# Performance work log

Measured on AMD Instinct MI355X. Metric: run time of the kernel, lower is better.

The kernel has to match this reference:

```python
import jax, jax.numpy as jnp
import numpy as np

WS = 7  # window_size
SHIFT = 3  # shift_size
NH = 4  # num_heads
EPS = 1e-5


def layer_norm(x, g, b):
    mu = jnp.mean(x, axis=-1, keepdims=True)
    var = jnp.mean(jnp.square(x - mu), axis=-1, keepdims=True)
    return (x - mu) * jax.lax.rsqrt(var + EPS) * g + b


def setup_inputs() -> dict:
    key = jax.random.key(0)
    ks = jax.random.split(key, 12)
    B, H, W, C = 64, 56, 56, 128
    hid = int(C * 3.0)
    s = lambda fan: 1.0 / np.sqrt(fan)
    return {
        "x": jax.random.normal(ks[0], (B, H * W, C), jnp.float32),
        "g1": jnp.ones((C,), jnp.float32),
        "be1": jnp.zeros((C,), jnp.float32),
        "Wqkv": jax.random.normal(ks[1], (3 * C, C), jnp.float32) * s(C),
        "bqkv": jnp.zeros((3 * C,), jnp.float32),
        "Wproj": jax.random.normal(ks[2], (C, C), jnp.float32) * s(C),
        "bproj": jnp.zeros((C,), jnp.float32),
        "g2": jnp.ones((C,), jnp.float32),
        "be2": jnp.zeros((C,), jnp.float32),
        "Wm1": jax.random.normal(ks[3], (hid, C), jnp.float32) * s(C),
        "bm1": jnp.zeros((hid,), jnp.float32),
        "Wm2": jax.random.normal(ks[4], (C, hid), jnp.float32) * s(hid),
        "bm2": jnp.zeros((C,), jnp.float32),
        "H": 56,
        "W": 56,
    }


def reference(x, g1, be1, Wqkv, bqkv, Wproj, bproj, g2, be2, Wm1, bm1, Wm2, bm2, H, W):
    B, L, C = x.shape
    shortcut = x
    h = layer_norm(x, g1, be1).reshape(B, H, W, C)
    if SHIFT > 0:
        h = jnp.roll(h, shift=(-SHIFT, -SHIFT), axis=(1, 2))
    pad_h = (WS - H % WS) % WS
    pad_w = (WS - W % WS) % WS
    if pad_h or pad_w:
        h = jnp.pad(h, ((0, 0), (0, pad_h), (0, pad_w), (0, 0)))
    Hp, Wp = H + pad_h, W + pad_w
    # window partition: [B*nW, WS*WS, C]
    h = h.reshape(B, Hp // WS, WS, Wp // WS, WS, C)
    h = h.transpose(0, 1, 3, 2, 4, 5).reshape(-1, WS * WS, C)
    # windowed attention (mask=None, matching original)
    Bw, N, _ = h.shape
    d = C // NH
    qkv = (h @ Wqkv.T + bqkv).reshape(Bw, N, 3, NH, d).transpose(2, 0, 3, 1, 4)
    q, k, v = qkv[0], qkv[1], qkv[2]  # [Bw, NH, N, d]
    attn = jax.nn.softmax(jnp.einsum('whnd,whmd->whnm', q, k) * (d ** -0.5), axis=-1)
    o = jnp.einsum('whnm,whmd->whnd', attn, v).transpose(0, 2, 1, 3).reshape(Bw, N, C)
    o = o @ Wproj.T + bproj
    # window reverse
    o = o.reshape(B, Hp // WS, Wp // WS, WS, WS, C)
    o = o.transpose(0, 1, 3, 2, 4, 5).reshape(B, Hp, Wp, C)
    if pad_h or pad_w:
        o = o[:, :H, :W, :]
    if SHIFT > 0:
        o = jnp.roll(o, shift=(SHIFT, SHIFT), axis=(1, 2))
    h = shortcut + o.reshape(B, H * W, C)
    # MLP with residual
    m = layer_norm(h, g2, be2)
    m = jax.nn.gelu(m @ Wm1.T + bm1, approximate=False) @ Wm2.T + bm2
    return h + m
```

## Files before the change

### kernel.cpp

```cpp
#include <hip/hip_runtime.h>
#include <hip/hip_bf16.h>
#include <cstdint>

typedef short bf16x8 __attribute__((ext_vector_type(8)));
typedef float f32x4 __attribute__((ext_vector_type(4)));

constexpr int Bn = 64, Hn = 56, Wn = 56, Cn = 128, Ln = 3136;
constexpr int NWIN = 4096;
constexpr int NTOK = 49;
constexpr int Mtot = NWIN * NTOK;
constexpr int HID = 384;
constexpr int SHIFT_ = 3;

__device__ __forceinline__ float bf2f(short s) {
  union { uint32_t u; float f; } c; c.u = ((uint32_t)(uint16_t)s) << 16; return c.f;
}
__device__ __forceinline__ short f2bf(float f) {
  union { float f; uint32_t u; } c; c.f = f;
  uint32_t r = (c.u + 0x7FFFu + ((c.u >> 16) & 1u)) >> 16;
  return (short)r;
}
__device__ __forceinline__ float wred(float v) {
  #pragma unroll
  for (int o = 32; o > 0; o >>= 1) v += __shfl_xor(v, o);
  return v;
}

__device__ __forceinline__ size_t plain_off(int m, int l15) {
  int win = m / NTOK, tok = m - win * NTOK;
  int b = win >> 6, wi = win & 63;
  int hr = (wi >> 3) * 7 + tok / 7 + SHIFT_; if (hr >= Hn) hr -= Hn;
  int wr = (wi & 7) * 7 + tok % 7 + SHIFT_;  if (wr >= Wn) wr -= Wn;
  return (size_t)(b * Ln + hr * Wn + wr) * Cn + l15;
}

__global__ void k_cvt4(const float* __restrict__ s0, const float* __restrict__ s1,
                       const float* __restrict__ s2, const float* __restrict__ s3,
                       short* __restrict__ d0, short* __restrict__ d1,
                       short* __restrict__ d2, short* __restrict__ d3) {
  int i = blockIdx.x * 256 + threadIdx.x;
  if (i < 49152) d0[i] = f2bf(s0[i]);
  else if (i < 65536) d1[i - 49152] = f2bf(s1[i - 49152]);
  else if (i < 114688) d2[i - 65536] = f2bf(s2[i - 65536]);
  else if (i < 163840) d3[i - 114688] = f2bf(s3[i - 114688]);
}

__global__ __launch_bounds__(256) void k_ln1(const float* __restrict__ x,
                                             const float* __restrict__ g,
                                             const float* __restrict__ be,
                                             short* __restrict__ out) {
  int wave = threadIdx.x >> 6, lane = threadIdx.x & 63;
  int row = blockIdx.x * 4 + wave;
  int win = row / NTOK, tok = row % NTOK;
  int b = win >> 6, wi = win & 63;
  int wh = wi >> 3, ww = wi & 7;
  int hr = wh * 7 + tok / 7;
  int wr = ww * 7 + tok % 7;
  int hs = hr + SHIFT_; if (hs >= Hn) hs -= Hn;
  int ws2 = wr + SHIFT_; if (ws2 >= Wn) ws2 -= Wn;
  const float* xr = x + (size_t)(b * Ln + hs * Wn + ws2) * Cn;
  float2 v = *(const float2*)(xr + lane * 2);
  float sum = wred(v.x + v.y);
  float sq  = wred(v.x * v.x + v.y * v.y);
  float mean = sum * (1.f / Cn);
  float var  = sq * (1.f / Cn) - mean * mean;
  float rstd = rsqrtf(var + 1e-5f);
  int c0 = lane * 2;
  short2 o;
  o.x = f2bf((v.x - mean) * rstd * g[c0]     + be[c0]);
  o.y = f2bf((v.y - mean) * rstd * g[c0 + 1] + be[c0 + 1]);
  *(short2*)(out + (size_t)row * Cn + c0) = o;
}

__global__ __launch_bounds__(512) void k_qkvg(const short* __restrict__ A,
                                              const short* __restrict__ W,
                                              const float* __restrict__ bias,
                                              short* __restrict__ outB) {
  __shared__ __attribute__((aligned(16))) short sW[64 * 128];
  const int t = threadIdx.x;
  const int wave = t >> 6, lane = t & 63;
  const int l15 = lane & 15, gq = lane >> 4;
  const int m_base = blockIdx.x * 128;
  const int wrow = wave * 16;
  const int kb = gq * 8;

  bf16x8 af[4];
  #pragma unroll
  for (int s = 0; s < 4; ++s)
    af[s] = *(const bf16x8*)(A + (size_t)(m_base + wrow + l15) * Cn + s * 32 + kb);

  short* b0[4];
  #pragma unroll
  for (int r = 0; r < 4; ++r) {
    int m = m_base + wrow + 4 * gq + r;
    int win = m / NTOK, tok = m - win * NTOK;
    b0[r] = outB + ((size_t)win * 3 * NTOK + tok) * Cn + l15;
  }

  #pragma unroll
  for (int nb = 0; nb < 6; ++nb) {
    __syncthreads();
    #pragma unroll
    for (int i = 0; i < 2; ++i) {
      int idx = i * 512 + t;
      int n = idx >> 4, gr = idx & 15;
      *(bf16x8*)(&sW[n * 128 + ((gr ^ (n & 7)) << 3)]) =
          *(const bf16x8*)(W + (size_t)(nb * 64 + n) * Cn + gr * 8);
    }
    __syncthreads();

    f32x4 acc[4];
    #pragma unroll
    for (int tt = 0; tt < 4; ++tt) acc[tt] = (f32x4){0.f, 0.f, 0.f, 0.f};
    #pragma unroll
    for (int s = 0; s < 4; ++s) {
      #pragma unroll
      for (int tt = 0; tt < 4; ++tt) {
        bf16x8 bfr = *(const bf16x8*)(&sW[(tt * 16 + l15) * 128 +
                                          (((s * 4 + gq) ^ (l15 & 7)) << 3)]);
        acc[tt] = __builtin_amdgcn_mfma_f32_16x16x32_bf16(af[s], bfr, acc[tt], 0, 0, 0);
      }
    }

    #pragma unroll
    for (int tt = 0; tt < 4; ++tt) {
      const int colc = nb * 64 + tt * 16;
      float bv = bias[colc + l15];
      #pragma unroll
      for (int r = 0; r < 4; ++r) {
        float v = acc[tt][r] + bv;
        b0[r][((colc >> 7) * NTOK * Cn) + (colc & 127)] = f2bf(v);
      }
    }
  }
}

__global__ __launch_bounds__(512) void k_mlp(const short* __restrict__ A,
                                             const short* __restrict__ W1,
                                             const float* __restrict__ b1,
                                             const short* __restrict__ W2,
                                             const float* __restrict__ b2,
                                             float* __restrict__ outF) {
  __shared__ __attribute__((aligned(16))) short sW1[64 * 128];
  __shared__ __attribute__((aligned(16))) short sW2[128 * 64];
  __shared__ __attribute__((aligned(16))) short sAct[128 * 64];
  const int t = threadIdx.x;
  const int wave = t >> 6, lane = t & 63;
  const int l15 = lane & 15, gq = lane >> 4;
  const int m_base = blockIdx.x * 128;
  const int wrow = wave * 16;
  const int kb = gq * 8;

  bf16x8 af[4];
  #pragma unroll
  for (int s = 0; s < 4; ++s)
    af[s] = *(const bf16x8*)(A + (size_t)(m_base + wrow + l15) * Cn + s * 32 + kb);

  f32x4 acc2[8];
  #pragma unroll
  for (int tt = 0; tt < 8; ++tt) acc2[tt] = (f32x4){0.f, 0.f, 0.f, 0.f};

  for (int nb = 0; nb < 6; ++nb) {
    __syncthreads();
    #pragma unroll
    for (int i = 0; i < 2; ++i) {
      int idx = i * 512 + t;
      int n = idx >> 4, gr = idx & 15;
      *(bf16x8*)(&sW1[n * 128 + ((gr ^ (n & 7)) << 3)]) =
          *(const bf16x8*)(W1 + (size_t)(nb * 64 + n) * Cn + gr * 8);
    }
    #pragma unroll
    for (int i = 0; i < 2; ++i) {
      int idx = i * 512 + t;
      int n = idx >> 3, gr = idx & 7;
      *(bf16x8*)(&sW2[n * 64 + ((gr ^ (n & 7)) << 3)]) =
          *(const bf16x8*)(W2 + (size_t)n * HID + nb * 64 + gr * 8);
    }
    __syncthreads();

    f32x4 acc1[4];
    #pragma unroll
    for (int tt = 0; tt < 4; ++tt) acc1[tt] = (f32x4){0.f, 0.f, 0.f, 0.f};
    #pragma unroll
    for (int s = 0; s < 4; ++s) {
      #pragma unroll
      for (int tt = 0; tt < 4; ++tt) {
        bf16x8 bfr = *(const bf16x8*)(&sW1[(tt * 16 + l15) * 128 +
                                           (((s * 4 + gq) ^ (l15 & 7)) << 3)]);
        acc1[tt] = __builtin_amdgcn_mfma_f32_16x16x32_bf16(af[s], bfr, acc1[tt], 0, 0, 0);
      }
    }
    #pragma unroll
    for (int tt = 0; tt < 4; ++tt) {
      float bb = b1[nb * 64 + tt * 16 + l15];
      #pragma unroll
      for (int r = 0; r < 4; ++r) {
        float v = acc1[tt][r] + bb;
        float e = __expf(-1.702f * v);
        float gg = v * __builtin_amdgcn_rcpf(1.f + e);
        int arow = wrow + 4 * gq + r;
        int col = tt * 16 + l15;
        sAct[arow * 64 + (((col >> 3) ^ (arow & 7)) << 3) + (col & 7)] = f2bf(gg);
      }
    }
    bf16x8 af2[2];
    #pragma unroll
    for (int sl = 0; sl < 2; ++sl)
      af2[sl] = *(const bf16x8*)(&sAct[(wrow + l15) * 64 +
                                       (((sl * 4 + gq) ^ (l15 & 7)) << 3)]);
    #pragma unroll
    for (int sl = 0; sl < 2; ++sl) {
      #pragma unroll
      for (int tt = 0; tt < 8; ++tt) {
        bf16x8 bfr = *(const bf16x8*)(&sW2[(tt * 16 + l15) * 64 +
                                           (((sl * 4 + gq) ^ (l15 & 7)) << 3)]);
        acc2[tt] = __builtin_amdgcn_mfma_f32_16x16x32_bf16(af2[sl], bfr, acc2[tt], 0, 0, 0);
      }
    }
  }

  float bb[8];
  #pragma unroll
  for (int tt = 0; tt < 8; ++tt) bb[tt] = b2[tt * 16 + l15];
  #pragma unroll
  for (int r = 0; r < 4; ++r) {
    int m = m_base + wrow + 4 * gq + r;
    float* p = outF + (size_t)m * Cn + l15;
    #pragma unroll
    for (int tt = 0; tt < 8; ++tt)
      p[tt * 16] = p[tt * 16] + acc2[tt][r] + bb[tt];
  }
}

__global__ __launch_bounds__(256) void k_proj(const short* __restrict__ A,
                                              const short* __restrict__ W,
                                              const float* __restrict__ bias,
                                              const float* __restrict__ x,
                                              const float* __restrict__ g2,
                                              const float* __restrict__ be2,
                                              float* __restrict__ hOut,
                                              short* __restrict__ lnOut) {
  __shared__ __attribute__((aligned(16))) short ldsW[128 * 128];
  const int t = threadIdx.x;
  const int wave = t >> 6, lane = t & 63;
  const int l15 = lane & 15, g = lane >> 4;
  const int m_base = blockIdx.x * 64 + wave * 16;
  const int kb = g * 8;

  size_t off[4];
  float xv[4][8];
  #pragma unroll
  for (int r = 0; r < 4; ++r) {
    int m = m_base + 4 * g + r;
    off[r] = plain_off(m, l15);
    #pragma unroll
    for (int c = 0; c < 8; ++c) xv[r][c] = x[off[r] + c * 16];
  }

  float bv[8], gv[8], bev[8];
  #pragma unroll
  for (int c = 0; c < 8; ++c) {
    bv[c] = bias[c * 16 + l15]; gv[c] = g2[c * 16 + l15]; bev[c] = be2[c * 16 + l15];
  }

  const int arow = m_base + l15;
  const int awin = arow / NTOK, atok = arow - awin * NTOK;
  const short* abase = A + (size_t)awin * 3 * NTOK * Cn + (size_t)atok * Cn;
  bf16x8 af[4];
  #pragma unroll
  for (int s = 0; s < 4; ++s)
    af[s] = *(const bf16x8*)(abase + s * 32 + kb);

  #pragma unroll
  for (int i = 0; i < 8; ++i) {
    int idx = i * 256 + t;
    int n = idx >> 4, gr = idx & 15;
    *(bf16x8*)(&ldsW[n * 128 + ((gr ^ (n & 7)) << 3)]) =
        *(const bf16x8*)(W + (size_t)n * Cn + gr * 8);
  }
  __syncthreads();

  f32x4 acc[8];
  #pragma unroll
  for (int tt = 0; tt < 8; ++tt) acc[tt] = (f32x4){0.f, 0.f, 0.f, 0.f};
  #pragma unroll
  for (int s = 0; s < 4; ++s) {
    #pragma unroll
    for (int tt = 0; tt < 8; ++tt) {
      int row = tt * 16 + l15;
      bf16x8 bfr = *(const bf16x8*)(&ldsW[row * 128 + (((s * 4 + g) ^ (l15 & 7)) << 3)]);
      acc[tt] = __builtin_amdgcn_mfma_f32_16x16x32_bf16(af[s], bfr, acc[tt], 0, 0, 0);
    }
  }

  #pragma unroll
  for (int r = 0; r < 4; ++r) {
    float hv[8];
    float s1 = 0.f, s2 = 0.f;
    #pragma unroll
    for (int tt = 0; tt < 8; ++tt) {
      hv[tt] = acc[tt][r] + bv[tt] + xv[r][tt];
      s1 += hv[tt];
      s2 += hv[tt] * hv[tt];
    }
    #pragma unroll
    for (int o = 8; o >= 1; o >>= 1) { s1 += __shfl_xor(s1, o); s2 += __shfl_xor(s2, o); }
    float mean = s1 * (1.f / Cn);
    float var  = s2 * (1.f / Cn) - mean * mean;
    float rstd = rsqrtf(var + 1e-5f);
    #pragma unroll
    for (int tt = 0; tt < 8; ++tt) {
      hOut[off[r] + tt * 16] = hv[tt];
      lnOut[off[r] + tt * 16] = f2bf((hv[tt] - mean) * rstd * gv[tt] + bev[tt]);
    }
  }
}

__global__ __launch_bounds__(256, 3) void k_attn(const short* __restrict__ qkv,
                                                 short* __restrict__ out) {
  __shared__ __attribute__((aligned(16))) short sVT[8192];
  __shared__ __attribute__((aligned(16))) short sP[4][4096];
  const int t = threadIdx.x;
  const int wave = t >> 6, lane = t & 63;
  const int l15 = lane & 15, g = lane >> 4;
  const int h = wave;
  const int win = blockIdx.x;
  const short* baseQ = qkv + (size_t)win * 3 * NTOK * Cn;
  const short* baseK = baseQ + NTOK * Cn;
  const short* baseV = baseK + NTOK * Cn;

  for (int i = t; i < NTOK * 16; i += 256) {
    int j = i >> 4, cb = (i & 15) * 8;
    int jj = j >> 3, u = j & 7;
    bf16x8 v = *(const bf16x8*)(baseV + (size_t)j * Cn + cb);
    #pragma unroll
    for (int uu = 0; uu < 8; ++uu) {
      int c = cb + uu;
      sVT[(c >> 4) * 1024 + (c & 15) * 64 + ((jj ^ (c & 7)) << 3) + u] = v[uu];
    }
  }
  for (int i = t; i < 128 * 15; i += 256) {
    int c = i / 15, j = 49 + i % 15;
    sVT[(c >> 4) * 1024 + (c & 15) * 64 + (((j >> 3) ^ (c & 7)) << 3) + (j & 7)] = 0;
  }

  bf16x8 aq[4], bk[4];
  #pragma unroll
  for (int mi = 0; mi < 4; ++mi)
    aq[mi] = *(const bf16x8*)(baseQ + (size_t)(mi * 16 + l15) * Cn + h * 32 + g * 8);
  #pragma unroll
  for (int ni = 0; ni < 4; ++ni)
    bk[ni] = *(const bf16x8*)(baseK + (size_t)(ni * 16 + l15) * Cn + h * 32 + g * 8);

  f32x4 s[4][4];
  #pragma unroll
  for (int mi = 0; mi < 4; ++mi)
    #pragma unroll
    for (int ni = 0; ni < 4; ++ni) {
      s[mi][ni] = (f32x4){0.f, 0.f, 0.f, 0.f};
      s[mi][ni] = __builtin_amdgcn_mfma_f32_16x16x32_bf16(aq[mi], bk[ni], s[mi][ni], 0, 0, 0);
    }

  const float SC = 0.17677669529663687f;
  #pragma unroll
  for (int mi = 0; mi < 4; ++mi) {
    #pragma unroll
    for (int r = 0; r < 4; ++r) {
      float a0 = s[mi][0][r] * SC, a1 = s[mi][1][r] * SC, a2 = s[mi][2][r] * SC;
      float a3 = (l15 == 0) ? s[mi][3][r] * SC : -1e30f;
      float m = fmaxf(fmaxf(a0, a1), fmaxf(a2, a3));
      #pragma unroll
      for (int o = 8; o >= 1; o >>= 1) m = fmaxf(m, __shfl_xor(m, o));
      float e0 = __expf(a0 - m), e1 = __expf(a1 - m), e2 = __expf(a2 - m);
      float e3 = (l15 == 0) ? __expf(a3 - m) : 0.f;
      float ss = e0 + e1 + e2 + e3;
      #pragma unroll
      for (int o = 8; o >= 1; o >>= 1) ss += __shfl_xor(ss, o);
      float inv = 1.f / ss;
      int rr = 4 * g + r;
      float ee[4] = {e0, e1, e2, e3};
      #pragma unroll
      for (int ni = 0; ni < 4; ++ni) {
        int col = 16 * ni + l15;
        sP[wave][(mi * 2 + (col >> 5)) * 512 + rr * 32 + (((col >> 3) & 3) * 8) + (col & 7)]
            = f2bf(ee[ni] * inv);
      }
    }
  }

  __syncthreads();

  f32x4 o_[4][2];
  #pragma unroll
  for (int mi = 0; mi < 4; ++mi)
    #pragma unroll
    for (int ni = 0; ni < 2; ++ni) o_[mi][ni] = (f32x4){0.f, 0.f, 0.f, 0.f};

  #pragma unroll
  for (int ks = 0; ks < 2; ++ks) {
    bf16x8 bv[2];
    #pragma unroll
    for (int ni = 0; ni < 2; ++ni)
      bv[ni] = *(const bf16x8*)(&sVT[(h * 2 + ni) * 1024 + l15 * 64 +
                                     (((ks * 4 + g) ^ (l15 & 7)) << 3)]);
    #pragma unroll
    for (int mi = 0; mi < 4; ++mi) {
      bf16x8 ap = *(const bf16x8*)(&sP[wave][(mi * 2 + ks) * 512 + l15 * 32 + g * 8]);
      #pragma unroll
      for (int ni = 0; ni < 2; ++ni)
        o_[mi][ni] = __builtin_amdgcn_mfma_f32_16x16x32_bf16(ap, bv[ni], o_[mi][ni], 0, 0, 0);
    }
  }

  #pragma unroll
  for (int mi = 0; mi < 4; ++mi) {
    #pragma unroll
    for (int r = 0; r < 4; ++r) {
      int i = 16 * mi + 4 * g + r;
      if (i < NTOK) {
        short* orow = out + ((size_t)win * 3 * NTOK + i) * Cn + h * 32;
        #pragma unroll
        for (int ni = 0; ni < 2; ++ni)
          orow[16 * ni + l15] = f2bf(o_[mi][ni][r]);
      }
    }
  }
}

extern "C" void kernel_launch(void* const* d_in, const int* in_sizes, int n_in,
                              void* d_out, int out_size, void* d_ws, size_t ws_size,
                              hipStream_t stream) {
  const float* x     = (const float*)d_in[0];
  const float* g1    = (const float*)d_in[1];
  const float* be1   = (const float*)d_in[2];
  const float* Wqkv  = (const float*)d_in[3];
  const float* bqkv  = (const float*)d_in[4];
  const float* Wproj = (const float*)d_in[5];
  const float* bproj = (const float*)d_in[6];
  const float* g2    = (const float*)d_in[7];
  const float* be2   = (const float*)d_in[8];
  const float* Wm1   = (const float*)d_in[9];
  const float* bm1   = (const float*)d_in[10];
  const float* Wm2   = (const float*)d_in[11];
  const float* bm2   = (const float*)d_in[12];
  float* out = (float*)d_out;

  char* ws = (char*)d_ws;
  size_t SA = (size_t)Mtot * Cn * 2;
  size_t SB = (size_t)Mtot * HID * 2;
  short* bufA = (short*)ws;
  short* bufB = (short*)(ws + SA);
  short* wq = (short*)(ws + SA + SB);
  short* wp = wq + 384 * 128;
  short* w1 = wp + 128 * 128;
  short* w2 = w1 + 384 * 128;

  k_cvt4<<<640, 256, 0, stream>>>(Wqkv, Wproj, Wm1, Wm2, wq, wp, w1, w2);

  k_ln1<<<Mtot / 4, 256, 0, stream>>>(x, g1, be1, bufA);
  k_qkvg<<<Mtot / 128, 512, 0, stream>>>(bufA, wq, bqkv, bufB);
  k_attn<<<NWIN, 256, 0, stream>>>(bufB, bufB);
  k_proj<<<Mtot / 64, 256, 0, stream>>>(bufB, wp, bproj, x, g2, be2, out, bufA);
  k_mlp<<<Mtot / 128, 512, 0, stream>>>(bufA, w1, bm1, w2, bm2, out);
}
```

Measured before the change: 322.1 us.

## Fuse projection, residual, LayerNorm2 and MLP into one kernel

Merges the attention output projection (with residual add and second LayerNorm) into the MLP kernel. The normalized activations stay in LDS and the residual stays in registers, so the fp32 h tensor and the bf16 LN tensor no longer make a round trip through global memory. The block now needs 80 KB of LDS and more registers (hv[4][8]), which may lower occupancy.

```diff
diff --git a/kernel.cpp b/kernel.cpp
--- a/kernel.cpp
+++ b/kernel.cpp
@@ -135,15 +135,23 @@
   }
 }
 
-__global__ __launch_bounds__(512) void k_mlp(const short* __restrict__ A,
-                                             const short* __restrict__ W1,
-                                             const float* __restrict__ b1,
-                                             const short* __restrict__ W2,
-                                             const float* __restrict__ b2,
-                                             float* __restrict__ outF) {
-  __shared__ __attribute__((aligned(16))) short sW1[64 * 128];
-  __shared__ __attribute__((aligned(16))) short sW2[128 * 64];
-  __shared__ __attribute__((aligned(16))) short sAct[128 * 64];
+__global__ __launch_bounds__(512) void k_projmlp(const short* __restrict__ A,
+                                                 const short* __restrict__ Wp,
+                                                 const float* __restrict__ bp,
+                                                 const float* __restrict__ x,
+                                                 const float* __restrict__ g2,
+                                                 const float* __restrict__ be2,
+                                                 const short* __restrict__ W1,
+                                                 const float* __restrict__ b1,
+                                                 const short* __restrict__ W2,
+                                                 const float* __restrict__ b2,
+                                                 float* __restrict__ outF) {
+  __shared__ __attribute__((aligned(16))) short lds[40960];
+  short* sWp  = lds;
+  short* sLn  = lds;
+  short* sW1  = lds + 16384;
+  short* sW2  = lds + 24576;
+  short* sAct = lds + 32768;
   const int t = threadIdx.x;
   const int wave = t >> 6, lane = t & 63;
   const int l15 = lane & 15, gq = lane >> 4;
@@ -151,10 +159,82 @@
   const int wrow = wave * 16;
   const int kb = gq * 8;
 
+  size_t off[4];
+  float xv[4][8];
+  #pragma unroll
+  for (int r = 0; r < 4; ++r) {
+    int m = m_base + wrow + 4 * gq + r;
+    off[r] = plain_off(m, l15);
+    #pragma unroll
+    for (int c = 0; c < 8; ++c) xv[r][c] = x[off[r] + c * 16];
+  }
+  float bpv[8], gv[8], bev[8];
+  #pragma unroll
+  for (int c = 0; c < 8; ++c) {
+    bpv[c] = bp[c * 16 + l15]; gv[c] = g2[c * 16 + l15]; bev[c] = be2[c * 16 + l15];
+  }
+
+  const int arow = m_base + wrow + l15;
+  const int awin = arow / NTOK, atok = arow - awin * NTOK;
+  const short* abase = A + (size_t)awin * 3 * NTOK * Cn + (size_t)atok * Cn;
   bf16x8 af[4];
   #pragma unroll
   for (int s = 0; s < 4; ++s)
-    af[s] = *(const bf16x8*)(A + (size_t)(m_base + wrow + l15) * Cn + s * 32 + kb);
+    af[s] = *(const bf16x8*)(abase + s * 32 + kb);
+
+  #pragma unroll
+  for (int i = 0; i < 4; ++i) {
+    int idx = i * 512 + t;
+    int n = idx >> 4, gr = idx & 15;
+    *(bf16x8*)(&sWp[n * 128 + ((gr ^ (n & 7)) << 3)]) =
+        *(const bf16x8*)(Wp + (size_t)n * Cn + gr * 8);
+  }
+  __syncthreads();
+
+  f32x4 acc[8];
+  #pragma unroll
+  for (int tt = 0; tt < 8; ++tt) acc[tt] = (f32x4){0.f, 0.f, 0.f, 0.f};
+  #pragma unroll
+  for (int s = 0; s < 4; ++s) {
+    #pragma unroll
+    for (int tt = 0; tt < 8; ++tt) {
+      int row = tt * 16 + l15;
+      bf16x8 bfr = *(const bf16x8*)(&sWp[row * 128 + (((s * 4 + gq) ^ (l15 & 7)) << 3)]);
+      acc[tt] = __builtin_amdgcn_mfma_f32_16x16x32_bf16(af[s], bfr, acc[tt], 0, 0, 0);
+    }
+  }
+
+  __syncthreads();
+
+  float hv[4][8];
+  #pragma unroll
+  for (int r = 0; r < 4; ++r) {
+    float s1 = 0.f, s2 = 0.f;
+    #pragma unroll
+    for (int tt = 0; tt < 8; ++tt) {
+      hv[r][tt] = acc[tt][r] + bpv[tt] + xv[r][tt];
+      s1 += hv[r][tt];
+      s2 += hv[r][tt] * hv[r][tt];
+    }
+    #pragma unroll
+    for (int o = 8; o >= 1; o >>= 1) { s1 += __shfl_xor(s1, o); s2 += __shfl_xor(s2, o); }
+    float mean = s1 * (1.f / Cn);
+    float var  = s2 * (1.f / Cn) - mean * mean;
+    float rstd = rsqrtf(var + 1e-5f);
+    int arw = wrow + 4 * gq + r;
+    #pragma unroll
+    for (int tt = 0; tt < 8; ++tt) {
+      int col = tt * 16 + l15;
+      sLn[arw * 128 + (((col >> 3) ^ (arw & 7)) << 3) + (col & 7)]
+          = f2bf((hv[r][tt] - mean) * rstd * gv[tt] + bev[tt]);
+    }
+  }
+
+  bf16x8 afm[4];
+  #pragma unroll
+  for (int s = 0; s < 4; ++s)
+    afm[s] = *(const bf16x8*)(&sLn[(wrow + l15) * 128 +
+                                   (((s * 4 + gq) ^ (l15 & 7)) << 3)]);
 
   f32x4 acc2[8];
   #pragma unroll
@@ -187,7 +267,7 @@
       for (int tt = 0; tt < 4; ++tt) {
         bf16x8 bfr = *(const bf16x8*)(&sW1[(tt * 16 + l15) * 128 +
                                            (((s * 4 + gq) ^ (l15 & 7)) << 3)]);
-        acc1[tt] = __builtin_amdgcn_mfma_f32_16x16x32_bf16(af[s], bfr, acc1[tt], 0, 0, 0);
+        acc1[tt] = __builtin_amdgcn_mfma_f32_16x16x32_bf16(afm[s], bfr, acc1[tt], 0, 0, 0);
       }
     }
     #pragma unroll
@@ -198,9 +278,9 @@
         float v = acc1[tt][r] + bb;
         float e = __expf(-1.702f * v);
         float gg = v * __builtin_amdgcn_rcpf(1.f + e);
-        int arow = wrow + 4 * gq + r;
+        int arw = wrow + 4 * gq + r;
         int col = tt * 16 + l15;
-        sAct[arow * 64 + (((col >> 3) ^ (arow & 7)) << 3) + (col & 7)] = f2bf(gg);
+        sAct[arw * 64 + (((col >> 3) ^ (arw & 7)) << 3) + (col & 7)] = f2bf(gg);
       }
     }
     bf16x8 af2[2];
@@ -219,100 +299,14 @@
     }
   }
 
-  float bb[8];
-  #pragma unroll
-  for (int tt = 0; tt < 8; ++tt) bb[tt] = b2[tt * 16 + l15];
+  float b2v[8];
+  #pragma unroll
+  for (int tt = 0; tt < 8; ++tt) b2v[tt] = b2[tt * 16 + l15];
   #pragma unroll
   for (int r = 0; r < 4; ++r) {
-    int m = m_base + wrow + 4 * gq + r;
-    float* p = outF + (size_t)m * Cn + l15;
     #pragma unroll
     for (int tt = 0; tt < 8; ++tt)
-      p[tt * 16] = p[tt * 16] + acc2[tt][r] + bb[tt];
-  }
-}
-
-__global__ __launch_bounds__(256) void k_proj(const short* __restrict__ A,
-                                              const short* __restrict__ W,
-                                              const float* __restrict__ bias,
-                                              const float* __restrict__ x,
-                                              const float* __restrict__ g2,
-                                              const float* __restrict__ be2,
-                                              float* __restrict__ hOut,
-                                              short* __restrict__ lnOut) {
-  __shared__ __attribute__((aligned(16))) short ldsW[128 * 128];
-  const int t = threadIdx.x;
-  const int wave = t >> 6, lane = t & 63;
-  const int l15 = lane & 15, g = lane >> 4;
-  const int m_base = blockIdx.x * 64 + wave * 16;
-  const int kb = g * 8;
-
-  size_t off[4];
-  float xv[4][8];
-  #pragma unroll
-  for (int r = 0; r < 4; ++r) {
-    int m = m_base + 4 * g + r;
-    off[r] = plain_off(m, l15);
-    #pragma unroll
-    for (int c = 0; c < 8; ++c) xv[r][c] = x[off[r] + c * 16];
-  }
-
-  float bv[8], gv[8], bev[8];
-  #pragma unroll
-  for (int c = 0; c < 8; ++c) {
-    bv[c] = bias[c * 16 + l15]; gv[c] = g2[c * 16 + l15]; bev[c] = be2[c * 16 + l15];
-  }
-
-  const int arow = m_base + l15;
-  const int awin = arow / NTOK, atok = arow - awin * NTOK;
-  const short* abase = A + (size_t)awin * 3 * NTOK * Cn + (size_t)atok * Cn;
-  bf16x8 af[4];
-  #pragma unroll
-  for (int s = 0; s < 4; ++s)
-    af[s] = *(const bf16x8*)(abase + s * 32 + kb);
-
-  #pragma unroll
-  for (int i = 0; i < 8; ++i) {
-    int idx = i * 256 + t;
-    int n = idx >> 4, gr = idx & 15;
-    *(bf16x8*)(&ldsW[n * 128 + ((gr ^ (n & 7)) << 3)]) =
-        *(const bf16x8*)(W + (size_t)n * Cn + gr * 8);
-  }
-  __syncthreads();
-
-  f32x4 acc[8];
-  #pragma unroll
-  for (int tt = 0; tt < 8; ++tt) acc[tt] = (f32x4){0.f, 0.f, 0.f, 0.f};
-  #pragma unroll
-  for (int s = 0; s < 4; ++s) {
-    #pragma unroll
-    for (int tt = 0; tt < 8; ++tt) {
-      int row = tt * 16 + l15;
-      bf16x8 bfr = *(const bf16x8*)(&ldsW[row * 128 + (((s * 4 + g) ^ (l15 & 7)) << 3)]);
-      acc[tt] = __builtin_amdgcn_mfma_f32_16x16x32_bf16(af[s], bfr, acc[tt], 0, 0, 0);
-    }
-  }
-
-  #pragma unroll
-  for (int r = 0; r < 4; ++r) {
-    float hv[8];
-    float s1 = 0.f, s2 = 0.f;
-    #pragma unroll
-    for (int tt = 0; tt < 8; ++tt) {
-      hv[tt] = acc[tt][r] + bv[tt] + xv[r][tt];
-      s1 += hv[tt];
-      s2 += hv[tt] * hv[tt];
-    }
-    #pragma unroll
-    for (int o = 8; o >= 1; o >>= 1) { s1 += __shfl_xor(s1, o); s2 += __shfl_xor(s2, o); }
-    float mean = s1 * (1.f / Cn);
-    float var  = s2 * (1.f / Cn) - mean * mean;
-    float rstd = rsqrtf(var + 1e-5f);
-    #pragma unroll
-    for (int tt = 0; tt < 8; ++tt) {
-      hOut[off[r] + tt * 16] = hv[tt];
-      lnOut[off[r] + tt * 16] = f2bf((hv[tt] - mean) * rstd * gv[tt] + bev[tt]);
-    }
+      outF[off[r] + tt * 16] = hv[r][tt] + acc2[tt][r] + b2v[tt];
   }
 }
 
@@ -460,6 +454,6 @@
   k_ln1<<<Mtot / 4, 256, 0, stream>>>(x, g1, be1, bufA);
   k_qkvg<<<Mtot / 128, 512, 0, stream>>>(bufA, wq, bqkv, bufB);
   k_attn<<<NWIN, 256, 0, stream>>>(bufB, bufB);
-  k_proj<<<Mtot / 64, 256, 0, stream>>>(bufB, wp, bproj, x, g2, be2, out, bufA);
-  k_mlp<<<Mtot / 128, 512, 0, stream>>>(bufA, w1, bm1, w2, bm2, out);
-}
+  k_projmlp<<<Mtot / 128, 512, 0, stream>>>(bufB, wp, bproj, x, g2, be2,
+                                            w1, bm1, w2, bm2, out);
+}
```

After: 316.4 us. About the same (-1.7%).
